# Kernel optimization log

Measured on AMD Instinct MI355X. Metric: run time of the kernel, lower is better.

Reference implementation:

```python
import jax, jax.numpy as jnp
import numpy as np

STEPS = 10          # points in t_grid -> STEPS-1 RK4 intervals
TRACE_STEPS = 2     # Hutchinson probes per dynamics eval
T_FINAL = 1.0
CLAMP = 100.0


def odefun(t, z, W1, b1, tw1, W2, b2):
    # time-conditioned 2-layer tanh MLP (canonical FFJORD dynamics)
    h = jnp.tanh(z @ W1 + b1 + t * tw1)
    return h @ W2 + b2


def setup_inputs() -> dict:
    key = jax.random.key(0)
    B, D, H = 2048, 512, 1024
    ks = jax.random.split(key, 4)
    s1 = 1.0 / np.sqrt(D)
    s2 = 1.0 / np.sqrt(H)
    return {
        "x": jax.random.normal(ks[0], (B, D), jnp.float32),
        "W1": jax.random.normal(ks[1], (D, H), jnp.float32) * s1,
        "b1": jnp.zeros((H,), jnp.float32),
        "tw1": jax.random.normal(ks[2], (H,), jnp.float32) * 0.1,
        "W2": jax.random.normal(ks[3], (H, D), jnp.float32) * s2,
        "b2": jnp.zeros((D,), jnp.float32),
    }


def reference(x, W1, b1, tw1, W2, b2):
    params = (W1, b1, tw1, W2, b2)
    B, D = x.shape

    def divergence_estimate(t, z, e):
        # torch detaches z before the grad call -> stop_gradient here
        z_sg = jax.lax.stop_gradient(z)
        f, vjp_fn = jax.vjp(lambda zz: odefun(t, zz, *params), z_sg)
        etf = vjp_fn(e)[0]                      # e^T J  (Hutchinson probe)
        return f, jnp.sum(etf * e, axis=-1)     # [B]

    def augmented_dynamics(t, state, key):
        z = state[:, :-1]                        # [B, D]
        div_est = jnp.zeros((B,), state.dtype)
        f_z = None
        for i in range(TRACE_STEPS):             # small fixed loop
            e = jax.random.randint(jax.random.fold_in(key, i), z.shape, 0, 2).astype(z.dtype) * 2.0 - 1.0
            f_z, div = divergence_estimate(t, z, e)
            div_est = div_est + div
        div_est = jnp.clip(div_est / TRACE_STEPS, -CLAMP, CLAMP)
        return jnp.concatenate([f_z, -div_est[:, None]], axis=-1)

    t_grid = jnp.linspace(0.0, T_FINAL, STEPS)
    state0 = jnp.concatenate([x, jnp.zeros((B, 1), x.dtype)], axis=-1)  # [B, D+1]

    def step(carry, t01):
        state, key = carry
        t0, t1 = t01[0], t01[1]
        dt = t1 - t0
        key, k1k, k2k, k3k, k4k = jax.random.split(key, 5)
        # torchdiffeq 'rk4' = Kutta's 3/8-rule variant (rk4_alt_step_func)
        k1 = augmented_dynamics(t0, state, k1k)
        k2 = augmented_dynamics(t0 + dt / 3.0, state + dt * k1 / 3.0, k2k)
        k3 = augmented_dynamics(t0 + dt * 2.0 / 3.0, state + dt * (k2 - k1 / 3.0), k3k)
        k4 = augmented_dynamics(t1, state + dt * (k1 - k2 + k3), k4k)
        state = state + (k1 + 3.0 * (k2 + k3) + k4) * dt * 0.125
        return (state, key), None

    t_pairs = jnp.stack([t_grid[:-1], t_grid[1:]], axis=-1)  # [STEPS-1, 2]
    (state, _), _ = jax.lax.scan(step, (state0, jax.random.key(1234)), t_pairs)

    rep, probsolve = state[:, :-1], state[:, -1]
    logprob = -0.5 * jnp.sum(rep * rep, axis=-1) + probsolve
    return rep, logprob
```

## Files before the change

kernel.cpp:

```cpp
#include <hip/hip_runtime.h>
#include <stdint.h>


#define B_N 2048
#define D_N 512
#define H_N 1024
#define BD (B_N * D_N)

typedef unsigned short u16;
typedef __attribute__((ext_vector_type(8))) short s16x8;
typedef __attribute__((ext_vector_type(4))) float f32x4;

typedef __attribute__((address_space(1))) const uint32_t ga_u32;
typedef __attribute__((address_space(3))) uint32_t ls_u32;

#if __has_builtin(__builtin_amdgcn_alignbit)
#define ROTL32(x, r) __builtin_amdgcn_alignbit((x), (x), 32 - (r))
#else
#define ROTL32(x, r) (((x) << (r)) | ((x) >> (32 - (r))))
#endif

__device__ __forceinline__ u16 f2bf(float f) {
  union { float f; uint32_t u; } c; c.f = f;
  uint32_t r = c.u + 0x7FFFu + ((c.u >> 16) & 1u);
  return (u16)(r >> 16);
}
__device__ __forceinline__ float fast_tanh(float v) {
  float e = __expf(2.0f * fabsf(v));
  float t = 1.0f - 2.0f / (e + 1.0f);
  return copysignf(t, v);
}

struct U2 { uint32_t x, y; };

__device__ __forceinline__ U2 tf2x32(uint32_t k0, uint32_t k1, uint32_t x0, uint32_t x1) {
  uint32_t k2 = k0 ^ k1 ^ 0x1BD11BDAu;
#define RND(r) { x0 += x1; x1 = ROTL32(x1, r); x1 ^= x0; }
  x0 += k0; x1 += k1;
  RND(13) RND(15) RND(26) RND(6)
  x0 += k1; x1 += k2 + 1u;
  RND(17) RND(29) RND(16) RND(24)
  x0 += k2; x1 += k0 + 2u;
  RND(13) RND(15) RND(26) RND(6)
  x0 += k0; x1 += k1 + 3u;
  RND(17) RND(29) RND(16) RND(24)
  x0 += k1; x1 += k2 + 4u;
  RND(13) RND(15) RND(26) RND(6)
  x0 += k2; x1 += k0 + 5u;
#undef RND
  U2 r; r.x = x0; r.y = x1; return r;
}

__global__ void k_keysched(uint32_t* __restrict__ ekeys) {
  if (threadIdx.x != 0 || blockIdx.x != 0) return;
  uint32_t kx = 0u, ky = 1234u;
  for (int s = 0; s < 9; ++s) {
    for (int st = 0; st < 4; ++st) {
      U2 kst = tf2x32(kx, ky, 0u, (uint32_t)(st + 1));
      for (int pr = 0; pr < 2; ++pr) {
        U2 fo = tf2x32(kst.x, kst.y, 0u, (uint32_t)pr);
        U2 k2 = tf2x32(fo.x, fo.y, 0u, 1u);
        ekeys[(s * 4 + st) * 4 + pr * 2 + 0] = k2.x;
        ekeys[(s * 4 + st) * 4 + pr * 2 + 1] = k2.y;
      }
    }
    U2 c = tf2x32(kx, ky, 0u, 0u);
    kx = c.x; ky = c.y;
  }
}

__global__ void k_init(const float* __restrict__ x, float* __restrict__ z, u16* __restrict__ zin,
                       float* __restrict__ lp, float* __restrict__ d0, float* __restrict__ d1,
                       uint32_t* __restrict__ barv) {
  int i = blockIdx.x * 256 + threadIdx.x;
  if (i < BD) { float v = x[i]; z[i] = v; zin[i] = f2bf(v); }
  if (i < B_N) { lp[i] = 0.f; d0[i] = 0.f; d1[i] = 0.f; }
  if (i < 1024) barv[i] = 0u;
}

__global__ void k_cvtT(const float* __restrict__ src, u16* __restrict__ dst, int R, int C) {
  int i = blockIdx.x * 256 + threadIdx.x;
  if (i >= R * C) return;
  int c = i / R, r = i - c * R;
  dst[i] = f2bf(src[(size_t)r * C + c]);
}
__global__ void k_cvt(const float* __restrict__ src, u16* __restrict__ dst, int n) {
  int i = blockIdx.x * 256 + threadIdx.x;
  if (i < n) dst[i] = f2bf(src[i]);
}

__global__ void k_sentinel(float* __restrict__ out, int n) {
  int i = blockIdx.x * 256 + threadIdx.x;
  if (i < n) out[i] = 12345.0f;
}

__device__ __forceinline__ void slab_bar(uint32_t* ctr, uint32_t tgt) {
  asm volatile("s_waitcnt vmcnt(0)" ::: "memory");
  __syncthreads();
  if (threadIdx.x == 0) {
    __hip_atomic_fetch_add(ctr, 1u, __ATOMIC_RELAXED, __HIP_MEMORY_SCOPE_AGENT);
    while (__hip_atomic_load(ctr, __ATOMIC_RELAXED, __HIP_MEMORY_SCOPE_AGENT) < tgt)
      __builtin_amdgcn_s_sleep(1);
  }
  __syncthreads();
}

__global__ __launch_bounds__(256, 1)
void k_fused(const uint32_t* __restrict__ keys, u16* __restrict__ ebf,
             u16* __restrict__ zin,
             const u16* __restrict__ W1T, const u16* __restrict__ W2b, const u16* __restrict__ W2T,
             const float* __restrict__ b1v, const float* __restrict__ tw1v, const float* __restrict__ b2v,
             float* __restrict__ z, float* __restrict__ ACC, float* __restrict__ T,
             u16* __restrict__ hbuf,
             float* __restrict__ lp, float* __restrict__ div0, float* __restrict__ div1,
             uint32_t* __restrict__ barv, float* __restrict__ outp) {
  __shared__ u16 S[4][14336];
  const int tid = threadIdx.x, wave = tid >> 6, lane = tid & 63;
  const int xcd = blockIdx.x & 7, idx = blockIdx.x >> 3;
  const int bm = xcd * 4 + (idx >> 3);
  const int bh = idx & 7;
  const int row0 = bm * 64;
  const int wm = wave >> 1, wn = wave & 1, r16 = lane & 15, q = lane >> 4;
  const int srow = lane >> 2;
  const int scol = (((lane & 3) ^ ((srow >> 1) & 3))) * 8;
  const int cqa = (q ^ ((r16 >> 1) & 3)) * 8;

  uint32_t* ctr = barv + bm * 32;
  uint32_t tgt = 0;

  auto egen_unit = [&](int stg, int u) {
    const int probe = u >> 10, unit = u & 1023;
    const uint32_t p0 = (uint32_t)(bm * 32768 + unit * 32);
    uint32_t k0 = keys[stg * 4 + probe * 2], k1 = keys[stg * 4 + probe * 2 + 1];
    uint4* dst = (uint4*)(ebf + (size_t)(stg & 3) * (2 * (size_t)BD) + (size_t)probe * BD + (size_t)p0);
#pragma unroll
    for (int g = 0; g < 4; ++g) {
      uint32_t pr[4];
#pragma unroll
      for (int h = 0; h < 4; ++h) {
        uint32_t c0 = p0 + g * 8 + h * 2;
        U2 r0 = tf2x32(k0, k1, 0u, c0);
        U2 r1 = tf2x32(k0, k1, 0u, c0 + 1u);
        pr[h] = (((r0.x ^ r0.y) & 1u) ? 0x3F80u : 0xBF80u) |
                (((r1.x ^ r1.y) & 1u) ? 0x3F800000u : 0xBF800000u);
      }
      uint4 v; v.x = pr[0]; v.y = pr[1]; v.z = pr[2]; v.w = pr[3];
      dst[g] = v;
    }
  };

#pragma unroll
  for (int r = 0; r < 4; ++r) egen_unit(r, bh * 256 + tid);
  tgt += 8; slab_bar(ctr, tgt);

  for (int st = 0; st < 36; ++st) {
    const int s9 = st >> 2, rsub = st & 3;
    const float t0f = (float)s9 / 9.0f;
    const float t1f = (float)(s9 + 1) / 9.0f;
    const float dtt = t1f - t0f;
    const float tstage = (rsub == 0) ? t0f : (rsub == 1) ? (t0f + dtt / 3.0f)
                       : (rsub == 2) ? (t0f + dtt * 2.0f / 3.0f) : t1f;
    const float wdt = dtt * 0.125f * ((rsub == 1 || rsub == 2) ? 3.0f : 1.0f);

    {
      const u16* e0g = ebf + (size_t)(st & 3) * (2 * (size_t)BD);
      const u16* e1g = e0g + BD;
      const int col0 = bh * 128;

      f32x4 az[2][4], au0[2][4], au1[2][4], av0[2][4], av1[2][4];
#pragma unroll
      for (int i = 0; i < 2; ++i)
#pragma unroll
        for (int j = 0; j < 4; ++j) {
          az[i][j] = (f32x4){0,0,0,0}; au0[i][j] = (f32x4){0,0,0,0}; au1[i][j] = (f32x4){0,0,0,0};
          av0[i][j] = (f32x4){0,0,0,0}; av1[i][j] = (f32x4){0,0,0,0};
        }

      const u16* gp[7];
#pragma unroll
      for (int li = 0; li < 7; ++li) {
        const int s = li * 4 + wave;
        const u16* base;
        int row;
        if (s < 12) {
          const int mat = s >> 2;
          base = (mat == 0) ? zin : (mat == 1) ? e0g : e1g;
          row = row0 + (s & 3) * 16 + srow;
        } else {
          const int t = s - 12;
          base = (t < 8) ? W1T : W2b;
          row = col0 + (t & 7) * 16 + srow;
        }
        gp[li] = base + (size_t)row * 512 + scol;
      }

      auto stg1 = [&](int kt, int slot) {
        u16* b = &S[slot][0];
#pragma unroll
        for (int li = 0; li < 7; ++li)
          __builtin_amdgcn_global_load_lds((ga_u32*)(gp[li] + kt),
                                           (ls_u32*)(b + (li * 4 + wave) * 512), 16, 0, 1);
      };
      auto cmp1 = [&](int slot) {
        const u16* b = &S[slot][0];
        s16x8 zf[2], e0f[2], e1f[2], w1f[4], w2f[4];
#pragma unroll
        for (int i = 0; i < 2; ++i) {
          const int ao = (wm * 32 + i * 16 + r16) * 32 + cqa;
          zf[i]  = *(const s16x8*)(b + 0    + ao);
          e0f[i] = *(const s16x8*)(b + 2048 + ao);
          e1f[i] = *(const s16x8*)(b + 4096 + ao);
        }
#pragma unroll
        for (int j = 0; j < 4; ++j) {
          const int bo = (wn * 64 + j * 16 + r16) * 32 + cqa;
          w1f[j] = *(const s16x8*)(b + 6144  + bo);
          w2f[j] = *(const s16x8*)(b + 10240 + bo);
        }
#pragma unroll
        for (int i = 0; i < 2; ++i)
#pragma unroll
          for (int j = 0; j < 4; ++j) {
            az[i][j]  = __builtin_amdgcn_mfma_f32_16x16x32_bf16(zf[i],  w1f[j], az[i][j],  0, 0, 0);
            au0[i][j] = __builtin_amdgcn_mfma_f32_16x16x32_bf16(e0f[i], w1f[j], au0[i][j], 0, 0, 0);
            au1[i][j] = __builtin_amdgcn_mfma_f32_16x16x32_bf16(e1f[i], w1f[j], au1[i][j], 0, 0, 0);
            av0[i][j] = __builtin_amdgcn_mfma_f32_16x16x32_bf16(e0f[i], w2f[j], av0[i][j], 0, 0, 0);
            av1[i][j] = __builtin_amdgcn_mfma_f32_16x16x32_bf16(e1f[i], w2f[j], av1[i][j], 0, 0, 0);
          }
      };

      stg1(0, 0); stg1(32, 1); stg1(64, 2);
      for (int it = 0; it < 16; ++it) {
        if (it < 14)        asm volatile("s_waitcnt vmcnt(14)" ::: "memory");
        else if (it == 14)  asm volatile("s_waitcnt vmcnt(7)" ::: "memory");
        else                asm volatile("s_waitcnt vmcnt(0)" ::: "memory");
        __builtin_amdgcn_s_barrier();
        if (it + 3 < 16) stg1((it + 3) * 32, (it + 3) & 3);
        cmp1(it & 3);
      }

      float d0s[2][4], d1s[2][4];
#pragma unroll
      for (int i = 0; i < 2; ++i)
#pragma unroll
        for (int rr = 0; rr < 4; ++rr) { d0s[i][rr] = 0.f; d1s[i][rr] = 0.f; }

#pragma unroll
      for (int j = 0; j < 4; ++j) {
        const int gcol = col0 + wn * 64 + j * 16 + r16;
        const float colb = b1v[gcol] + tstage * tw1v[gcol];
#pragma unroll
        for (int i = 0; i < 2; ++i) {
          const int rbase = row0 + wm * 32 + i * 16 + q * 4;
#pragma unroll
          for (int rr = 0; rr < 4; ++rr) {
            float hv = fast_tanh(az[i][j][rr] + colb);
            hbuf[(size_t)(rbase + rr) * H_N + gcol] = f2bf(hv);
            float sd = 1.f - hv * hv;
            d0s[i][rr] += sd * au0[i][j][rr] * av0[i][j][rr];
            d1s[i][rr] += sd * au1[i][j][rr] * av1[i][j][rr];
          }
        }
      }
#pragma unroll
      for (int i = 0; i < 2; ++i)
#pragma unroll
        for (int rr = 0; rr < 4; ++rr) {
          float a = d0s[i][rr], bb = d1s[i][rr];
#pragma unroll
          for (int m = 1; m < 16; m <<= 1) { a += __shfl_xor(a, m); bb += __shfl_xor(bb, m); }
          if (r16 == 0) {
            int grow = row0 + wm * 32 + i * 16 + q * 4 + rr;
            atomicAdd(&div0[grow], a);
            atomicAdd(&div1[grow], bb);
          }
        }
    }
    tgt += 8; slab_bar(ctr, tgt);

    {
      const int col0 = bh * 64;
      u16* S3 = &S[0][0];

      f32x4 a3[2][2];
      a3[0][0] = (f32x4){0,0,0,0}; a3[0][1] = (f32x4){0,0,0,0};
      a3[1][0] = (f32x4){0,0,0,0}; a3[1][1] = (f32x4){0,0,0,0};

      const u16* gp3[2];
      gp3[0] = hbuf + (size_t)(row0 + wave * 16 + srow) * 1024 + scol;
      gp3[1] = W2T  + (size_t)(col0 + wave * 16 + srow) * 1024 + scol;

      auto stg3 = [&](int kt, int slot) {
        u16* b = S3 + slot * 4096;
        __builtin_amdgcn_global_load_lds((ga_u32*)(gp3[0] + kt),
                                         (ls_u32*)(b + wave * 512), 16, 0, 1);
        __builtin_amdgcn_global_load_lds((ga_u32*)(gp3[1] + kt),
                                         (ls_u32*)(b + 2048 + wave * 512), 16, 0, 1);
      };
      auto cmp3 = [&](int slot) {
        const u16* b = S3 + slot * 4096;
        s16x8 af[2], bf[2];
#pragma unroll
        for (int i = 0; i < 2; ++i)
          af[i] = *(const s16x8*)(b + (wm * 32 + i * 16 + r16) * 32 + cqa);
#pragma unroll
        for (int j = 0; j < 2; ++j)
          bf[j] = *(const s16x8*)(b + 2048 + (wn * 32 + j * 16 + r16) * 32 + cqa);
#pragma unroll
        for (int i = 0; i < 2; ++i)
#pragma unroll
          for (int j = 0; j < 2; ++j)
            a3[i][j] = __builtin_amdgcn_mfma_f32_16x16x32_bf16(af[i], bf[j], a3[i][j], 0, 0, 0);
      };

      stg3(0, 0); stg3(32, 1); stg3(64, 2);
      for (int it = 0; it < 32; ++it) {
        if (it < 30)        asm volatile("s_waitcnt vmcnt(4)" ::: "memory");
        else if (it == 30)  asm volatile("s_waitcnt vmcnt(2)" ::: "memory");
        else                asm volatile("s_waitcnt vmcnt(0)" ::: "memory");
        __builtin_amdgcn_s_barrier();
        if (it + 3 < 32) stg3((it + 3) * 32, (it + 3) & 3);
        cmp3(it & 3);
      }

      if (bh == 0 && tid < 64) {
        int b = row0 + tid;
        float c0 = __hip_atomic_load(&div0[b], __ATOMIC_RELAXED, __HIP_MEMORY_SCOPE_AGENT);
        float c1 = __hip_atomic_load(&div1[b], __ATOMIC_RELAXED, __HIP_MEMORY_SCOPE_AGENT);
        float c = 0.5f * (c0 + c1);
        c = fminf(fmaxf(c, -100.f), 100.f);
        lp[b] -= wdt * c;
        div0[b] = 0.f; div1[b] = 0.f;
      }

#pragma unroll
      for (int j = 0; j < 2; ++j) {
        const int gcol = col0 + wn * 32 + j * 16 + r16;
        const float cb = b2v[gcol];
#pragma unroll
        for (int i = 0; i < 2; ++i) {
          const int rbase = row0 + wm * 32 + i * 16 + q * 4;
#pragma unroll
          for (int rr = 0; rr < 4; ++rr) {
            const size_t idx2 = (size_t)(rbase + rr) * D_N + gcol;
            const float f = a3[i][j][rr] + cb;
            if (rsub == 0) {
              ACC[idx2] = dtt * 0.125f * f;
              T[idx2]   = dtt * f;
              zin[idx2] = f2bf(z[idx2] + dtt * f * (1.f / 3.f));
            } else if (rsub == 1) {
              float t_ = T[idx2];
              ACC[idx2] += 0.375f * dtt * f;
              zin[idx2] = f2bf(z[idx2] + dtt * f - t_ * (1.f / 3.f));
              T[idx2]   = t_ - dtt * f;
            } else if (rsub == 2) {
              ACC[idx2] += 0.375f * dtt * f;
              zin[idx2] = f2bf(z[idx2] + T[idx2] + dtt * f);
            } else {
              float zn = z[idx2] + ACC[idx2] + dtt * 0.125f * f;
              z[idx2]   = zn;
              zin[idx2] = f2bf(zn);
            }
          }
        }
      }

      if (st + 4 < 36) egen_unit(st + 4, bh * 256 + tid);
    }
    tgt += 8; slab_bar(ctr, tgt);
  }

#pragma unroll
  for (int rr = 0; rr < 2; ++rr) {
    const int b = bm * 64 + bh * 8 + wave * 2 + rr;
    const float* zr = z + (size_t)b * D_N + lane * 8;
    float4 v0 = *(const float4*)zr;
    float4 v1 = *(const float4*)(zr + 4);
    *(float4*)(outp + (size_t)b * D_N + lane * 8)     = v0;
    *(float4*)(outp + (size_t)b * D_N + lane * 8 + 4) = v1;
    float ss = v0.x*v0.x + v0.y*v0.y + v0.z*v0.z + v0.w*v0.w
             + v1.x*v1.x + v1.y*v1.y + v1.z*v1.z + v1.w*v1.w;
#pragma unroll
    for (int m = 1; m < 64; m <<= 1) ss += __shfl_xor(ss, m);
    if (lane == 0) {
      float lpv = __hip_atomic_load(&lp[b], __ATOMIC_RELAXED, __HIP_MEMORY_SCOPE_AGENT);
      outp[(size_t)BD + b] = -0.5f * ss + lpv;
    }
  }
}

extern "C" void kernel_launch(void* const* d_in, const int* in_sizes, int n_in,
                              void* d_out, int out_size, void* d_ws, size_t ws_size,
                              hipStream_t stream) {
  const float* x   = (const float*)d_in[0];
  const float* W1  = (const float*)d_in[1];
  const float* b1  = (const float*)d_in[2];
  const float* tw1 = (const float*)d_in[3];
  const float* W2  = (const float*)d_in[4];
  const float* b2  = (const float*)d_in[5];
  float* outp = (float*)d_out;

  const size_t NEEDED = (size_t)45 << 20;
  if (ws_size < NEEDED) {
    k_sentinel<<<(BD + B_N + 255) / 256, 256, 0, stream>>>(outp, BD + B_N);
    return;
  }
  char* w = (char*)d_ws;
  auto carve = [&](size_t bytes) { char* p = w; w += (bytes + 255) & ~(size_t)255; return p; };
  uint32_t* keys = (uint32_t*)carve(144 * sizeof(uint32_t));
  u16* ebf   = (u16*)carve((size_t)4 * 2 * BD * 2);
  float* z   = (float*)carve((size_t)BD * 4);
  float* ACC = (float*)carve((size_t)BD * 4);
  float* T   = (float*)carve((size_t)BD * 4);
  u16* zin   = (u16*)carve((size_t)BD * 2);
  u16* hbuf  = (u16*)carve((size_t)B_N * H_N * 2);
  u16* W1T   = (u16*)carve((size_t)H_N * D_N * 2);
  u16* W2b   = (u16*)carve((size_t)H_N * D_N * 2);
  u16* W2T   = (u16*)carve((size_t)D_N * H_N * 2);
  float* lp   = (float*)carve((size_t)B_N * 4);
  float* div0 = (float*)carve((size_t)B_N * 4);
  float* div1 = (float*)carve((size_t)B_N * 4);
  uint32_t* barv = (uint32_t*)carve(4096);

  k_keysched<<<1, 1, 0, stream>>>(keys);
  k_init<<<BD / 256, 256, 0, stream>>>(x, z, zin, lp, div0, div1, barv);
  k_cvtT<<<(D_N * H_N) / 256, 256, 0, stream>>>(W1, W1T, D_N, H_N);
  k_cvt <<<(H_N * D_N) / 256, 256, 0, stream>>>(W2, W2b, H_N * D_N);
  k_cvtT<<<(H_N * D_N) / 256, 256, 0, stream>>>(W2, W2T, H_N, D_N);

  k_fused<<<256, 256, 0, stream>>>(keys, ebf, zin, W1T, W2b, W2T, b1, tw1, b2,
                                   z, ACC, T, hbuf, lp, div0, div1, barv, outp);
}
```

Before: 1.452 ms.

## Keep RK4 state in registers and double K-step of the third GEMM stage

```diff
diff --git a/kernel.cpp b/kernel.cpp
--- a/kernel.cpp
+++ b/kernel.cpp
@@ -69,11 +69,11 @@
   }
 }
 
-__global__ void k_init(const float* __restrict__ x, float* __restrict__ z, u16* __restrict__ zin,
+__global__ void k_init(const float* __restrict__ x, u16* __restrict__ zin,
                        float* __restrict__ lp, float* __restrict__ d0, float* __restrict__ d1,
                        uint32_t* __restrict__ barv) {
   int i = blockIdx.x * 256 + threadIdx.x;
-  if (i < BD) { float v = x[i]; z[i] = v; zin[i] = f2bf(v); }
+  if (i < BD) zin[i] = f2bf(x[i]);
   if (i < B_N) { lp[i] = 0.f; d0[i] = 0.f; d1[i] = 0.f; }
   if (i < 1024) barv[i] = 0u;
 }
@@ -107,10 +107,9 @@
 
 __global__ __launch_bounds__(256, 1)
 void k_fused(const uint32_t* __restrict__ keys, u16* __restrict__ ebf,
-             u16* __restrict__ zin,
+             const float* __restrict__ x, u16* __restrict__ zin,
              const u16* __restrict__ W1T, const u16* __restrict__ W2b, const u16* __restrict__ W2T,
              const float* __restrict__ b1v, const float* __restrict__ tw1v, const float* __restrict__ b2v,
-             float* __restrict__ z, float* __restrict__ ACC, float* __restrict__ T,
              u16* __restrict__ hbuf,
              float* __restrict__ lp, float* __restrict__ div0, float* __restrict__ div1,
              uint32_t* __restrict__ barv, float* __restrict__ outp) {
@@ -128,6 +127,19 @@
   uint32_t* ctr = barv + bm * 32;
   uint32_t tgt = 0;
 
+  float zr_[2][2][4], ac_[2][2][4], tt_[2][2][4];
+#pragma unroll
+  for (int i = 0; i < 2; ++i)
+#pragma unroll
+    for (int j = 0; j < 2; ++j)
+#pragma unroll
+      for (int rr = 0; rr < 4; ++rr) {
+        const size_t idx2 = (size_t)(row0 + wm * 32 + i * 16 + q * 4 + rr) * D_N
+                          + bh * 64 + wn * 32 + j * 16 + r16;
+        zr_[i][j][rr] = x[idx2];
+        ac_[i][j][rr] = 0.f; tt_[i][j][rr] = 0.f;
+      }
+
   auto egen_unit = [&](int stg, int u) {
     const int probe = u >> 10, unit = u & 1023;
     const uint32_t p0 = (uint32_t)(bm * 32768 + unit * 32);
@@ -286,40 +298,46 @@
       a3[0][0] = (f32x4){0,0,0,0}; a3[0][1] = (f32x4){0,0,0,0};
       a3[1][0] = (f32x4){0,0,0,0}; a3[1][1] = (f32x4){0,0,0,0};
 
-      const u16* gp3[2];
-      gp3[0] = hbuf + (size_t)(row0 + wave * 16 + srow) * 1024 + scol;
-      gp3[1] = W2T  + (size_t)(col0 + wave * 16 + srow) * 1024 + scol;
+      const u16* gp3a = hbuf + (size_t)(row0 + wave * 16 + srow) * 1024 + scol;
+      const u16* gp3b = W2T  + (size_t)(col0 + wave * 16 + srow) * 1024 + scol;
 
       auto stg3 = [&](int kt, int slot) {
-        u16* b = S3 + slot * 4096;
-        __builtin_amdgcn_global_load_lds((ga_u32*)(gp3[0] + kt),
+        u16* b = S3 + slot * 8192;
+        __builtin_amdgcn_global_load_lds((ga_u32*)(gp3a + kt),
                                          (ls_u32*)(b + wave * 512), 16, 0, 1);
-        __builtin_amdgcn_global_load_lds((ga_u32*)(gp3[1] + kt),
+        __builtin_amdgcn_global_load_lds((ga_u32*)(gp3a + kt + 32),
                                          (ls_u32*)(b + 2048 + wave * 512), 16, 0, 1);
+        __builtin_amdgcn_global_load_lds((ga_u32*)(gp3b + kt),
+                                         (ls_u32*)(b + 4096 + wave * 512), 16, 0, 1);
+        __builtin_amdgcn_global_load_lds((ga_u32*)(gp3b + kt + 32),
+                                         (ls_u32*)(b + 6144 + wave * 512), 16, 0, 1);
       };
       auto cmp3 = [&](int slot) {
-        const u16* b = S3 + slot * 4096;
-        s16x8 af[2], bf[2];
-#pragma unroll
-        for (int i = 0; i < 2; ++i)
-          af[i] = *(const s16x8*)(b + (wm * 32 + i * 16 + r16) * 32 + cqa);
-#pragma unroll
-        for (int j = 0; j < 2; ++j)
-          bf[j] = *(const s16x8*)(b + 2048 + (wn * 32 + j * 16 + r16) * 32 + cqa);
-#pragma unroll
-        for (int i = 0; i < 2; ++i)
+        const u16* b = S3 + slot * 8192;
+#pragma unroll
+        for (int ks = 0; ks < 2; ++ks) {
+          s16x8 af[2], bf[2];
+#pragma unroll
+          for (int i = 0; i < 2; ++i)
+            af[i] = *(const s16x8*)(b + ks * 2048 + (wm * 32 + i * 16 + r16) * 32 + cqa);
 #pragma unroll
           for (int j = 0; j < 2; ++j)
-            a3[i][j] = __builtin_amdgcn_mfma_f32_16x16x32_bf16(af[i], bf[j], a3[i][j], 0, 0, 0);
+            bf[j] = *(const s16x8*)(b + 4096 + ks * 2048 + (wn * 32 + j * 16 + r16) * 32 + cqa);
+#pragma unroll
+          for (int i = 0; i < 2; ++i)
+#pragma unroll
+            for (int j = 0; j < 2; ++j)
+              a3[i][j] = __builtin_amdgcn_mfma_f32_16x16x32_bf16(af[i], bf[j], a3[i][j], 0, 0, 0);
+        }
       };
 
-      stg3(0, 0); stg3(32, 1); stg3(64, 2);
-      for (int it = 0; it < 32; ++it) {
-        if (it < 30)        asm volatile("s_waitcnt vmcnt(4)" ::: "memory");
-        else if (it == 30)  asm volatile("s_waitcnt vmcnt(2)" ::: "memory");
+      stg3(0, 0); stg3(64, 1); stg3(128, 2);
+      for (int it = 0; it < 16; ++it) {
+        if (it < 14)        asm volatile("s_waitcnt vmcnt(8)" ::: "memory");
+        else if (it == 14)  asm volatile("s_waitcnt vmcnt(4)" ::: "memory");
         else                asm volatile("s_waitcnt vmcnt(0)" ::: "memory");
         __builtin_amdgcn_s_barrier();
-        if (it + 3 < 32) stg3((it + 3) * 32, (it + 3) & 3);
+        if (it + 3 < 16) stg3((it + 3) * 64, (it + 3) & 3);
         cmp3(it & 3);
       }
 
@@ -345,20 +363,20 @@
             const size_t idx2 = (size_t)(rbase + rr) * D_N + gcol;
             const float f = a3[i][j][rr] + cb;
             if (rsub == 0) {
-              ACC[idx2] = dtt * 0.125f * f;
-              T[idx2]   = dtt * f;
-              zin[idx2] = f2bf(z[idx2] + dtt * f * (1.f / 3.f));
+              ac_[i][j][rr] = dtt * 0.125f * f;
+              tt_[i][j][rr] = dtt * f;
+              zin[idx2] = f2bf(zr_[i][j][rr] + dtt * f * (1.f / 3.f));
             } else if (rsub == 1) {
-              float t_ = T[idx2];
-              ACC[idx2] += 0.375f * dtt * f;
-              zin[idx2] = f2bf(z[idx2] + dtt * f - t_ * (1.f / 3.f));
-              T[idx2]   = t_ - dtt * f;
+              float t_ = tt_[i][j][rr];
+              ac_[i][j][rr] += 0.375f * dtt * f;
+              zin[idx2] = f2bf(zr_[i][j][rr] + dtt * f - t_ * (1.f / 3.f));
+              tt_[i][j][rr] = t_ - dtt * f;
             } else if (rsub == 2) {
-              ACC[idx2] += 0.375f * dtt * f;
-              zin[idx2] = f2bf(z[idx2] + T[idx2] + dtt * f);
+              ac_[i][j][rr] += 0.375f * dtt * f;
+              zin[idx2] = f2bf(zr_[i][j][rr] + tt_[i][j][rr] + dtt * f);
             } else {
-              float zn = z[idx2] + ACC[idx2] + dtt * 0.125f * f;
-              z[idx2]   = zn;
+              float zn = zr_[i][j][rr] + ac_[i][j][rr] + dtt * 0.125f * f;
+              zr_[i][j][rr] = zn;
               zin[idx2] = f2bf(zn);
             }
           }
@@ -371,21 +389,29 @@
   }
 
 #pragma unroll
-  for (int rr = 0; rr < 2; ++rr) {
-    const int b = bm * 64 + bh * 8 + wave * 2 + rr;
-    const float* zr = z + (size_t)b * D_N + lane * 8;
-    float4 v0 = *(const float4*)zr;
-    float4 v1 = *(const float4*)(zr + 4);
-    *(float4*)(outp + (size_t)b * D_N + lane * 8)     = v0;
-    *(float4*)(outp + (size_t)b * D_N + lane * 8 + 4) = v1;
-    float ss = v0.x*v0.x + v0.y*v0.y + v0.z*v0.z + v0.w*v0.w
-             + v1.x*v1.x + v1.y*v1.y + v1.z*v1.z + v1.w*v1.w;
-#pragma unroll
-    for (int m = 1; m < 64; m <<= 1) ss += __shfl_xor(ss, m);
-    if (lane == 0) {
-      float lpv = __hip_atomic_load(&lp[b], __ATOMIC_RELAXED, __HIP_MEMORY_SCOPE_AGENT);
-      outp[(size_t)BD + b] = -0.5f * ss + lpv;
+  for (int i = 0; i < 2; ++i) {
+#pragma unroll
+    for (int rr = 0; rr < 4; ++rr) {
+      const int grow = row0 + wm * 32 + i * 16 + q * 4 + rr;
+      float val = 0.f;
+#pragma unroll
+      for (int j = 0; j < 2; ++j) {
+        const int gcol = bh * 64 + wn * 32 + j * 16 + r16;
+        const float v = zr_[i][j][rr];
+        outp[(size_t)grow * D_N + gcol] = v;
+        val += v * v;
+      }
+#pragma unroll
+      for (int m = 1; m < 16; m <<= 1) val += __shfl_xor(val, m);
+      if (r16 == 0) atomicAdd(&div0[grow], val);
     }
+  }
+  tgt += 8; slab_bar(ctr, tgt);
+  if (bh == 0 && tid < 64) {
+    const int b = row0 + tid;
+    float ss = __hip_atomic_load(&div0[b], __ATOMIC_RELAXED, __HIP_MEMORY_SCOPE_AGENT);
+    float lpv = __hip_atomic_load(&lp[b], __ATOMIC_RELAXED, __HIP_MEMORY_SCOPE_AGENT);
+    outp[(size_t)BD + b] = -0.5f * ss + lpv;
   }
 }
 
@@ -409,9 +435,6 @@
   auto carve = [&](size_t bytes) { char* p = w; w += (bytes + 255) & ~(size_t)255; return p; };
   uint32_t* keys = (uint32_t*)carve(144 * sizeof(uint32_t));
   u16* ebf   = (u16*)carve((size_t)4 * 2 * BD * 2);
-  float* z   = (float*)carve((size_t)BD * 4);
-  float* ACC = (float*)carve((size_t)BD * 4);
-  float* T   = (float*)carve((size_t)BD * 4);
   u16* zin   = (u16*)carve((size_t)BD * 2);
   u16* hbuf  = (u16*)carve((size_t)B_N * H_N * 2);
   u16* W1T   = (u16*)carve((size_t)H_N * D_N * 2);
@@ -423,11 +446,11 @@
   uint32_t* barv = (uint32_t*)carve(4096);
 
   k_keysched<<<1, 1, 0, stream>>>(keys);
-  k_init<<<BD / 256, 256, 0, stream>>>(x, z, zin, lp, div0, div1, barv);
+  k_init<<<BD / 256, 256, 0, stream>>>(x, zin, lp, div0, div1, barv);
   k_cvtT<<<(D_N * H_N) / 256, 256, 0, stream>>>(W1, W1T, D_N, H_N);
   k_cvt <<<(H_N * D_N) / 256, 256, 0, stream>>>(W2, W2b, H_N * D_N);
   k_cvtT<<<(H_N * D_N) / 256, 256, 0, stream>>>(W2, W2T, H_N, D_N);
 
-  k_fused<<<256, 256, 0, stream>>>(keys, ebf, zin, W1T, W2b, W2T, b1, tw1, b2,
-                                   z, ACC, T, hbuf, lp, div0, div1, barv, outp);
-}
+  k_fused<<<256, 256, 0, stream>>>(keys, ebf, x, zin, W1T, W2b, W2T, b1, tw1, b2,
+                                   hbuf, lp, div0, div1, barv, outp);
+}
```

Result: slower. 1.718 ms (+18.3%).

## Double persistent grid to 512 blocks with narrower per-block column tiles

Applied to the files above, without the earlier changes.

```diff
diff --git a/kernel.cpp b/kernel.cpp
--- a/kernel.cpp
+++ b/kernel.cpp
@@ -105,7 +105,7 @@
   __syncthreads();
 }
 
-__global__ __launch_bounds__(256, 1)
+__global__ __launch_bounds__(256, 2)
 void k_fused(const uint32_t* __restrict__ keys, u16* __restrict__ ebf,
              u16* __restrict__ zin,
              const u16* __restrict__ W1T, const u16* __restrict__ W2b, const u16* __restrict__ W2T,
@@ -114,11 +114,11 @@
              u16* __restrict__ hbuf,
              float* __restrict__ lp, float* __restrict__ div0, float* __restrict__ div1,
              uint32_t* __restrict__ barv, float* __restrict__ outp) {
-  __shared__ u16 S[4][14336];
+  __shared__ u16 S[4][10240];
   const int tid = threadIdx.x, wave = tid >> 6, lane = tid & 63;
   const int xcd = blockIdx.x & 7, idx = blockIdx.x >> 3;
-  const int bm = xcd * 4 + (idx >> 3);
-  const int bh = idx & 7;
+  const int bm = xcd * 4 + (idx >> 4);
+  const int bh = idx & 15;
   const int row0 = bm * 64;
   const int wm = wave >> 1, wn = wave & 1, r16 = lane & 15, q = lane >> 4;
   const int srow = lane >> 2;
@@ -128,13 +128,13 @@
   uint32_t* ctr = barv + bm * 32;
   uint32_t tgt = 0;
 
-  auto egen_unit = [&](int stg, int u) {
-    const int probe = u >> 10, unit = u & 1023;
-    const uint32_t p0 = (uint32_t)(bm * 32768 + unit * 32);
+  auto egen_unit = [&](int stg, int t) {
+    const int probe = t >> 11, e16 = t & 2047;
+    const uint32_t p0 = (uint32_t)(bm * 32768 + e16 * 16);
     uint32_t k0 = keys[stg * 4 + probe * 2], k1 = keys[stg * 4 + probe * 2 + 1];
     uint4* dst = (uint4*)(ebf + (size_t)(stg & 3) * (2 * (size_t)BD) + (size_t)probe * BD + (size_t)p0);
 #pragma unroll
-    for (int g = 0; g < 4; ++g) {
+    for (int g = 0; g < 2; ++g) {
       uint32_t pr[4];
 #pragma unroll
       for (int h = 0; h < 4; ++h) {
@@ -151,7 +151,7 @@
 
 #pragma unroll
   for (int r = 0; r < 4; ++r) egen_unit(r, bh * 256 + tid);
-  tgt += 8; slab_bar(ctr, tgt);
+  tgt += 16; slab_bar(ctr, tgt);
 
   for (int st = 0; st < 36; ++st) {
     const int s9 = st >> 2, rsub = st & 3;
@@ -165,20 +165,20 @@
     {
       const u16* e0g = ebf + (size_t)(st & 3) * (2 * (size_t)BD);
       const u16* e1g = e0g + BD;
-      const int col0 = bh * 128;
-
-      f32x4 az[2][4], au0[2][4], au1[2][4], av0[2][4], av1[2][4];
+      const int col0 = bh * 64;
+
+      f32x4 az[2][2], au0[2][2], au1[2][2], av0[2][2], av1[2][2];
 #pragma unroll
       for (int i = 0; i < 2; ++i)
 #pragma unroll
-        for (int j = 0; j < 4; ++j) {
+        for (int j = 0; j < 2; ++j) {
           az[i][j] = (f32x4){0,0,0,0}; au0[i][j] = (f32x4){0,0,0,0}; au1[i][j] = (f32x4){0,0,0,0};
           av0[i][j] = (f32x4){0,0,0,0}; av1[i][j] = (f32x4){0,0,0,0};
         }
 
-      const u16* gp[7];
-#pragma unroll
-      for (int li = 0; li < 7; ++li) {
+      const u16* gp[5];
+#pragma unroll
+      for (int li = 0; li < 5; ++li) {
         const int s = li * 4 + wave;
         const u16* base;
         int row;
@@ -188,8 +188,8 @@
           row = row0 + (s & 3) * 16 + srow;
         } else {
           const int t = s - 12;
-          base = (t < 8) ? W1T : W2b;
-          row = col0 + (t & 7) * 16 + srow;
+          base = (t < 4) ? W1T : W2b;
+          row = col0 + (t & 3) * 16 + srow;
         }
         gp[li] = base + (size_t)row * 512 + scol;
       }
@@ -197,13 +197,13 @@
       auto stg1 = [&](int kt, int slot) {
         u16* b = &S[slot][0];
 #pragma unroll
-        for (int li = 0; li < 7; ++li)
+        for (int li = 0; li < 5; ++li)
           __builtin_amdgcn_global_load_lds((ga_u32*)(gp[li] + kt),
                                            (ls_u32*)(b + (li * 4 + wave) * 512), 16, 0, 1);
       };
       auto cmp1 = [&](int slot) {
         const u16* b = &S[slot][0];
-        s16x8 zf[2], e0f[2], e1f[2], w1f[4], w2f[4];
+        s16x8 zf[2], e0f[2], e1f[2], w1f[2], w2f[2];
 #pragma unroll
         for (int i = 0; i < 2; ++i) {
           const int ao = (wm * 32 + i * 16 + r16) * 32 + cqa;
@@ -212,15 +212,15 @@
           e1f[i] = *(const s16x8*)(b + 4096 + ao);
         }
 #pragma unroll
-        for (int j = 0; j < 4; ++j) {
-          const int bo = (wn * 64 + j * 16 + r16) * 32 + cqa;
-          w1f[j] = *(const s16x8*)(b + 6144  + bo);
-          w2f[j] = *(const s16x8*)(b + 10240 + bo);
+        for (int j = 0; j < 2; ++j) {
+          const int bo = (wn * 32 + j * 16 + r16) * 32 + cqa;
+          w1f[j] = *(const s16x8*)(b + 6144 + bo);
+          w2f[j] = *(const s16x8*)(b + 8192 + bo);
         }
 #pragma unroll
         for (int i = 0; i < 2; ++i)
 #pragma unroll
-          for (int j = 0; j < 4; ++j) {
+          for (int j = 0; j < 2; ++j) {
             az[i][j]  = __builtin_amdgcn_mfma_f32_16x16x32_bf16(zf[i],  w1f[j], az[i][j],  0, 0, 0);
             au0[i][j] = __builtin_amdgcn_mfma_f32_16x16x32_bf16(e0f[i], w1f[j], au0[i][j], 0, 0, 0);
             au1[i][j] = __builtin_amdgcn_mfma_f32_16x16x32_bf16(e1f[i], w1f[j], au1[i][j], 0, 0, 0);
@@ -231,8 +231,8 @@
 
       stg1(0, 0); stg1(32, 1); stg1(64, 2);
       for (int it = 0; it < 16; ++it) {
-        if (it < 14)        asm volatile("s_waitcnt vmcnt(14)" ::: "memory");
-        else if (it == 14)  asm volatile("s_waitcnt vmcnt(7)" ::: "memory");
+        if (it < 14)        asm volatile("s_waitcnt vmcnt(10)" ::: "memory");
+        else if (it == 14)  asm volatile("s_waitcnt vmcnt(5)" ::: "memory");
         else                asm volatile("s_waitcnt vmcnt(0)" ::: "memory");
         __builtin_amdgcn_s_barrier();
         if (it + 3 < 16) stg1((it + 3) * 32, (it + 3) & 3);
@@ -246,8 +246,8 @@
         for (int rr = 0; rr < 4; ++rr) { d0s[i][rr] = 0.f; d1s[i][rr] = 0.f; }
 
 #pragma unroll
-      for (int j = 0; j < 4; ++j) {
-        const int gcol = col0 + wn * 64 + j * 16 + r16;
+      for (int j = 0; j < 2; ++j) {
+        const int gcol = col0 + wn * 32 + j * 16 + r16;
         const float colb = b1v[gcol] + tstage * tw1v[gcol];
 #pragma unroll
         for (int i = 0; i < 2; ++i) {
@@ -276,52 +276,36 @@
           }
         }
     }
-    tgt += 8; slab_bar(ctr, tgt);
+    tgt += 16; slab_bar(ctr, tgt);
 
     {
-      const int col0 = bh * 64;
+      const int col0 = bh * 32;
       u16* S3 = &S[0][0];
 
-      f32x4 a3[2][2];
-      a3[0][0] = (f32x4){0,0,0,0}; a3[0][1] = (f32x4){0,0,0,0};
-      a3[1][0] = (f32x4){0,0,0,0}; a3[1][1] = (f32x4){0,0,0,0};
-
-      const u16* gp3[2];
-      gp3[0] = hbuf + (size_t)(row0 + wave * 16 + srow) * 1024 + scol;
-      gp3[1] = W2T  + (size_t)(col0 + wave * 16 + srow) * 1024 + scol;
+      f32x4 acc[2];
+      acc[0] = (f32x4){0,0,0,0}; acc[1] = (f32x4){0,0,0,0};
+
+      const u16* gp3a = hbuf + (size_t)(row0 + wave * 16 + srow) * 1024 + scol;
+      const u16* gp3b = W2T  + (size_t)(col0 + (wave & 1) * 16 + srow) * 1024 + scol;
 
       auto stg3 = [&](int kt, int slot) {
-        u16* b = S3 + slot * 4096;
-        __builtin_amdgcn_global_load_lds((ga_u32*)(gp3[0] + kt),
+        u16* b = S3 + slot * 3072;
+        __builtin_amdgcn_global_load_lds((ga_u32*)(gp3a + kt),
                                          (ls_u32*)(b + wave * 512), 16, 0, 1);
-        __builtin_amdgcn_global_load_lds((ga_u32*)(gp3[1] + kt),
-                                         (ls_u32*)(b + 2048 + wave * 512), 16, 0, 1);
+        if (wave < 2)
+          __builtin_amdgcn_global_load_lds((ga_u32*)(gp3b + kt),
+                                           (ls_u32*)(b + 2048 + wave * 512), 16, 0, 1);
       };
       auto cmp3 = [&](int slot) {
-        const u16* b = S3 + slot * 4096;
-        s16x8 af[2], bf[2];
-#pragma unroll
-        for (int i = 0; i < 2; ++i)
-          af[i] = *(const s16x8*)(b + (wm * 32 + i * 16 + r16) * 32 + cqa);
-#pragma unroll
-        for (int j = 0; j < 2; ++j)
-          bf[j] = *(const s16x8*)(b + 2048 + (wn * 32 + j * 16 + r16) * 32 + cqa);
-#pragma unroll
-        for (int i = 0; i < 2; ++i)
-#pragma unroll
-          for (int j = 0; j < 2; ++j)
-            a3[i][j] = __builtin_amdgcn_mfma_f32_16x16x32_bf16(af[i], bf[j], a3[i][j], 0, 0, 0);
+        const u16* b = S3 + slot * 3072;
+        s16x8 af  = *(const s16x8*)(b + (wave * 16 + r16) * 32 + cqa);
+        s16x8 bf0 = *(const s16x8*)(b + 2048 + r16 * 32 + cqa);
+        s16x8 bf1 = *(const s16x8*)(b + 2048 + (16 + r16) * 32 + cqa);
+        acc[0] = __builtin_amdgcn_mfma_f32_16x16x32_bf16(af, bf0, acc[0], 0, 0, 0);
+        acc[1] = __builtin_amdgcn_mfma_f32_16x16x32_bf16(af, bf1, acc[1], 0, 0, 0);
       };
 
       stg3(0, 0); stg3(32, 1); stg3(64, 2);
-      for (int it = 0; it < 32; ++it) {
-        if (it < 30)        asm volatile("s_waitcnt vmcnt(4)" ::: "memory");
-        else if (it == 30)  asm volatile("s_waitcnt vmcnt(2)" ::: "memory");
-        else                asm volatile("s_waitcnt vmcnt(0)" ::: "memory");
-        __builtin_amdgcn_s_barrier();
-        if (it + 3 < 32) stg3((it + 3) * 32, (it + 3) & 3);
-        cmp3(it & 3);
-      }
 
       if (bh == 0 && tid < 64) {
         int b = row0 + tid;
@@ -333,46 +317,57 @@
         div0[b] = 0.f; div1[b] = 0.f;
       }
 
+      for (int it = 0; it < 32; ++it) {
+        if (it < 30) {
+          if (wave < 2) asm volatile("s_waitcnt vmcnt(4)" ::: "memory");
+          else          asm volatile("s_waitcnt vmcnt(2)" ::: "memory");
+        } else if (it == 30) {
+          if (wave < 2) asm volatile("s_waitcnt vmcnt(2)" ::: "memory");
+          else          asm volatile("s_waitcnt vmcnt(1)" ::: "memory");
+        } else {
+          asm volatile("s_waitcnt vmcnt(0)" ::: "memory");
+        }
+        __builtin_amdgcn_s_barrier();
+        if (it + 3 < 32) stg3((it + 3) * 32, (it + 3) & 3);
+        cmp3(it & 3);
+      }
+
 #pragma unroll
       for (int j = 0; j < 2; ++j) {
-        const int gcol = col0 + wn * 32 + j * 16 + r16;
+        const int gcol = col0 + j * 16 + r16;
         const float cb = b2v[gcol];
-#pragma unroll
-        for (int i = 0; i < 2; ++i) {
-          const int rbase = row0 + wm * 32 + i * 16 + q * 4;
-#pragma unroll
-          for (int rr = 0; rr < 4; ++rr) {
-            const size_t idx2 = (size_t)(rbase + rr) * D_N + gcol;
-            const float f = a3[i][j][rr] + cb;
-            if (rsub == 0) {
-              ACC[idx2] = dtt * 0.125f * f;
-              T[idx2]   = dtt * f;
-              zin[idx2] = f2bf(z[idx2] + dtt * f * (1.f / 3.f));
-            } else if (rsub == 1) {
-              float t_ = T[idx2];
-              ACC[idx2] += 0.375f * dtt * f;
-              zin[idx2] = f2bf(z[idx2] + dtt * f - t_ * (1.f / 3.f));
-              T[idx2]   = t_ - dtt * f;
-            } else if (rsub == 2) {
-              ACC[idx2] += 0.375f * dtt * f;
-              zin[idx2] = f2bf(z[idx2] + T[idx2] + dtt * f);
-            } else {
-              float zn = z[idx2] + ACC[idx2] + dtt * 0.125f * f;
-              z[idx2]   = zn;
-              zin[idx2] = f2bf(zn);
-            }
+        const int rbase = row0 + wave * 16 + q * 4;
+#pragma unroll
+        for (int rr = 0; rr < 4; ++rr) {
+          const size_t idx2 = (size_t)(rbase + rr) * D_N + gcol;
+          const float f = acc[j][rr] + cb;
+          if (rsub == 0) {
+            ACC[idx2] = dtt * 0.125f * f;
+            T[idx2]   = dtt * f;
+            zin[idx2] = f2bf(z[idx2] + dtt * f * (1.f / 3.f));
+          } else if (rsub == 1) {
+            float t_ = T[idx2];
+            ACC[idx2] += 0.375f * dtt * f;
+            zin[idx2] = f2bf(z[idx2] + dtt * f - t_ * (1.f / 3.f));
+            T[idx2]   = t_ - dtt * f;
+          } else if (rsub == 2) {
+            ACC[idx2] += 0.375f * dtt * f;
+            zin[idx2] = f2bf(z[idx2] + T[idx2] + dtt * f);
+          } else {
+            float zn = z[idx2] + ACC[idx2] + dtt * 0.125f * f;
+            z[idx2]   = zn;
+            zin[idx2] = f2bf(zn);
           }
         }
       }
 
       if (st + 4 < 36) egen_unit(st + 4, bh * 256 + tid);
     }
-    tgt += 8; slab_bar(ctr, tgt);
+    tgt += 16; slab_bar(ctr, tgt);
   }
 
-#pragma unroll
-  for (int rr = 0; rr < 2; ++rr) {
-    const int b = bm * 64 + bh * 8 + wave * 2 + rr;
+  {
+    const int b = row0 + bh * 4 + wave;
     const float* zr = z + (size_t)b * D_N + lane * 8;
     float4 v0 = *(const float4*)zr;
     float4 v1 = *(const float4*)(zr + 4);
@@ -428,6 +423,6 @@
   k_cvt <<<(H_N * D_N) / 256, 256, 0, stream>>>(W2, W2b, H_N * D_N);
   k_cvtT<<<(H_N * D_N) / 256, 256, 0, stream>>>(W2, W2T, H_N, D_N);
 
-  k_fused<<<256, 256, 0, stream>>>(keys, ebf, zin, W1T, W2b, W2T, b1, tw1, b2,
+  k_fused<<<512, 256, 0, stream>>>(keys, ebf, zin, W1T, W2b, W2T, b1, tw1, b2,
                                    z, ACC, T, hbuf, lp, div0, div1, barv, outp);
 }
```

Measured after the change: 1.456 ms. No clear change (+0.3%).
